# Optimization experiments

Measured on AMD Instinct MI355X. Metric: run time of the kernel, lower is better.

The kernel has to match this reference:

```python
import jax, jax.numpy as jnp
import numpy as np

D_MODEL, D_STATE, D_CONV, EXPAND = 2048, 16, 4, 2
D_INNER = EXPAND * D_MODEL            # 4096
DT_RANK = -(-D_MODEL // 16)           # 128
B_SZ, L = 2, 1024


def setup_inputs() -> dict:
    key = jax.random.key(0)
    ks = jax.random.split(key, 10)
    s = 0.02
    return {
        "hidden_states": jax.random.normal(ks[0], (B_SZ, L, D_MODEL), jnp.float32),
        "in_proj_w": jax.random.normal(ks[1], (2 * D_INNER, D_MODEL), jnp.float32) * s,
        "conv_w": jax.random.normal(ks[2], (D_INNER, D_CONV), jnp.float32) * 0.1,
        "conv_b": jax.random.normal(ks[3], (D_INNER,), jnp.float32) * 0.1,
        "x_proj_w": jax.random.normal(ks[4], (DT_RANK + 2 * D_STATE, D_INNER), jnp.float32) * s,
        "dt_proj_w": jax.random.normal(ks[5], (D_INNER, DT_RANK), jnp.float32) * s,
        "dt_proj_b": jax.random.normal(ks[6], (D_INNER,), jnp.float32) * 0.1 - 4.0,
        "A": -jax.random.uniform(ks[7], (D_INNER, D_STATE), jnp.float32, 1.0, 16.0),
        "D": jnp.ones((D_INNER,), jnp.float32),
        "out_proj_w": jax.random.normal(ks[8], (D_MODEL, D_INNER), jnp.float32) * s,
    }


def _mamba_forward(hidden_states, in_proj_w, conv_w, conv_b, x_proj_w,
                   dt_proj_w, dt_proj_b, A, D, out_proj_w):
    # in_proj: [B,L,d_model] -> [B,L,2*d_inner]; chunk into x and gate
    proj = jnp.einsum('bld,ed->ble', hidden_states, in_proj_w)
    x, gate = jnp.split(proj, 2, axis=-1)            # each [B,L,d_inner]

    # depthwise causal conv1d over time + SiLU
    xc = x.transpose(0, 2, 1)                        # [B,d_inner,L]
    xc = jax.lax.conv_general_dilated(
        xc, conv_w[:, None, :],                      # kernel [d_inner,1,d_conv]
        window_strides=(1,), padding=[(D_CONV - 1, 0)],
        feature_group_count=D_INNER,
        dimension_numbers=('NCH', 'OIH', 'NCH'))
    xc = jax.nn.silu(xc + conv_b[None, :, None])
    xt = xc.transpose(0, 2, 1)                       # [B,L,d_inner]

    # x_proj -> (dt_rank, d_state, d_state)
    ssm = jnp.einsum('bld,ed->ble', xt, x_proj_w)
    ts, Bm, Cm = jnp.split(ssm, [DT_RANK, DT_RANK + D_STATE], axis=-1)
    dt = jnp.einsum('blr,dr->bld', ts, dt_proj_w)    # dt_proj (skip_bias_add)
    dt = jax.nn.softplus(dt + dt_proj_b)             # delta_softplus with bias

    # selective scan over time
    def step(state, inp):
        dt_t, x_t, B_t, C_t = inp                    # [B,di],[B,di],[B,ds],[B,ds]
        dA = jnp.exp(dt_t[..., None] * A)            # [B,d_inner,d_state]
        dBx = dt_t[..., None] * B_t[:, None, :] * x_t[..., None]
        state = state * dA + dBx
        y = jnp.einsum('bds,bs->bd', state, C_t)
        return state, y

    xs = (dt.transpose(1, 0, 2), xt.transpose(1, 0, 2),
          Bm.transpose(1, 0, 2), Cm.transpose(1, 0, 2))
    state0 = jnp.zeros((hidden_states.shape[0], D_INNER, D_STATE), jnp.float32)
    _, ys = jax.lax.scan(step, state0, xs)           # [L,B,d_inner]
    y = ys.transpose(1, 0, 2) + xt * D               # D skip connection
    y = y * jax.nn.silu(gate)                        # gating (z in selective scan)

    return jnp.einsum('bld,ed->ble', y, out_proj_w)  # out_proj -> [B,L,d_model]


def reference(hidden_states, in_proj_w, conv_w, conv_b, x_proj_w,
              dt_proj_w, dt_proj_b, A, D, out_proj_w):
    return _mamba_forward(hidden_states, in_proj_w, conv_w, conv_b, x_proj_w,
                          dt_proj_w, dt_proj_b, A, D, out_proj_w)
```

## Files before the change

kernel.cpp:

```cpp
#include <hip/hip_runtime.h>
#include <hip/hip_bf16.h>
#include <math.h>

#define B_SZ    2
#define LSEQ    1024
#define D_MODEL 2048
#define D_INNER 4096
#define D_STATE 16
#define DT_RANK 128
#define M_TOK   (B_SZ * LSEQ)
#define NCHUNK  16
#define LCHUNK  (LSEQ / NCHUNK)
#define LOG2E   1.4426950408889634f

typedef __attribute__((ext_vector_type(8))) short bf16x8;
typedef __attribute__((ext_vector_type(4))) float f32x4;

__device__ __forceinline__ float softplusf_(float x) {
    return fmaxf(x, 0.f) + log1pf(expf(-fabsf(x)));
}
__device__ __forceinline__ unsigned f2bf(float f) {
    union { float f; unsigned u; } v; v.f = f;
    const unsigned u = v.u;
    return (u + 0x7fffu + ((u >> 16) & 1u)) >> 16;
}
__device__ __forceinline__ float bf2f(unsigned u) {
    union { unsigned u; float f; } v; v.u = u << 16; return v.f;
}
__device__ __forceinline__ void gload16(const void* g, void* lds) {
    __builtin_amdgcn_global_load_lds(
        (const __attribute__((address_space(1))) void*)g,
        (__attribute__((address_space(3))) void*)lds, 16, 0, 0);
}
__device__ __forceinline__ float exp2fast(float x) {
    return __builtin_amdgcn_exp2f(x);
}
__device__ __forceinline__ float sigmoid2(float x) {
    return 1.f / (1.f + exp2fast(-x * LOG2E));
}

__global__ __launch_bounds__(512, 2)
void gemm256_1ph(const ushort* __restrict__ A, int lda,
                 const ushort* __restrict__ B, int ldb,
                 void* __restrict__ Cv, int ldc,
                 void* __restrict__ Cv2,
                 int K, int epi, size_t zstride)
{
    __shared__ ushort Lds[2][2][2][128 * 64];
    const int t    = threadIdx.x;
    const int bm   = blockIdx.y << 8, bn = blockIdx.x << 8;
    const int wave = t >> 6, lane = t & 63;
    const int wm   = wave >> 2;
    const int wn   = wave & 3;
    const int lr   = lane & 15, lh = lane >> 4;
    const int kper  = K / gridDim.z;
    const int kbase = blockIdx.z * kper;
    const int nkt   = kper >> 6;

    const ushort* gsA[2]; const ushort* gsB[2];
    int dof[2];
#pragma unroll
    for (int it = 0; it < 2; ++it) {
        const int flat = t + (it << 9);
        const int row  = flat >> 3, j = flat & 7;
        const int jj   = j ^ (row & 7);
        gsA[it] = A + (size_t)(bm + row) * lda + kbase + jj * 8;
        gsB[it] = B + (size_t)(bn + row) * ldb + kbase + jj * 8;
        dof[it] = flat << 3;
    }

#define STG_A(half, kt, db) do {                                            \
    _Pragma("unroll")                                                       \
    for (int it = 0; it < 2; ++it)                                          \
        gload16(gsA[it] + (size_t)((half) * 128) * lda + (kt) * 64,         \
                &Lds[db][0][half][dof[it]]);                                \
} while (0)
#define STG_B(half, kt, db) do {                                            \
    _Pragma("unroll")                                                       \
    for (int it = 0; it < 2; ++it)                                          \
        gload16(gsB[it] + (size_t)((half) * 128) * ldb + (kt) * 64,         \
                &Lds[db][1][half][dof[it]]);                                \
} while (0)
#define RD_A(db, half) do {                                                 \
    _Pragma("unroll")                                                       \
    for (int mi = 0; mi < 4; ++mi)                                          \
    _Pragma("unroll")                                                       \
    for (int kk = 0; kk < 2; ++kk) {                                        \
        const int row_ = wm * 64 + mi * 16 + lr;                            \
        const int ch_  = ((kk << 2) + lh) ^ (row_ & 7);                     \
        af[mi * 2 + kk] = *(const bf16x8*)((const char*)Lds[db][0][half]    \
                             + row_ * 128 + (ch_ << 4));                    \
    }                                                                       \
} while (0)
#define RD_B(db, half, dst) do {                                            \
    _Pragma("unroll")                                                       \
    for (int nj = 0; nj < 2; ++nj)                                          \
    _Pragma("unroll")                                                       \
    for (int kk = 0; kk < 2; ++kk) {                                        \
        const int row_ = wn * 32 + nj * 16 + lr;                            \
        const int ch_  = ((kk << 2) + lh) ^ (row_ & 7);                     \
        dst[nj * 2 + kk] = *(const bf16x8*)((const char*)Lds[db][1][half]   \
                             + row_ * 128 + (ch_ << 4));                    \
    }                                                                       \
} while (0)
#define MFMA_PAIR(qa, qb, bfa, bfb) do {                                    \
    _Pragma("unroll")                                                       \
    for (int kk = 0; kk < 2; ++kk) {                                        \
        _Pragma("unroll")                                                   \
        for (int mi = 0; mi < 4; ++mi)                                      \
        _Pragma("unroll")                                                   \
        for (int nj = 0; nj < 2; ++nj)                                      \
            acc[qa][mi][nj] = __builtin_amdgcn_mfma_f32_16x16x32_bf16(      \
                af[mi * 2 + kk], bfa[nj * 2 + kk], acc[qa][mi][nj], 0, 0, 0);\
        _Pragma("unroll")                                                   \
        for (int mi = 0; mi < 4; ++mi)                                      \
        _Pragma("unroll")                                                   \
        for (int nj = 0; nj < 2; ++nj)                                      \
            acc[qb][mi][nj] = __builtin_amdgcn_mfma_f32_16x16x32_bf16(      \
                af[mi * 2 + kk], bfb[nj * 2 + kk], acc[qb][mi][nj], 0, 0, 0);\
    }                                                                       \
} while (0)

    f32x4 acc[4][4][2];
#pragma unroll
    for (int q = 0; q < 4; ++q)
#pragma unroll
        for (int i = 0; i < 4; ++i)
#pragma unroll
            for (int j = 0; j < 2; ++j) {
                acc[q][i][j][0] = 0.f; acc[q][i][j][1] = 0.f;
                acc[q][i][j][2] = 0.f; acc[q][i][j][3] = 0.f;
            }

    bf16x8 af[8], bf0[4], bf1[4];

    STG_A(0, 0, 0); STG_B(0, 0, 0); STG_B(1, 0, 0); STG_A(1, 0, 0);
    asm volatile("s_waitcnt vmcnt(0)" ::: "memory");
    __builtin_amdgcn_s_barrier();

    for (int kt = 0; kt < nkt; ++kt) {
        const int db = kt & 1;
        RD_A(db, 0); RD_B(db, 0, bf0); RD_B(db, 1, bf1);
        if (kt + 1 < nkt) {
            STG_A(0, kt + 1, db ^ 1); STG_B(0, kt + 1, db ^ 1);
            STG_B(1, kt + 1, db ^ 1); STG_A(1, kt + 1, db ^ 1);
        }
        MFMA_PAIR(0, 1, bf0, bf1);
        RD_A(db, 1);
        MFMA_PAIR(2, 3, bf1, bf0);
        asm volatile("s_waitcnt vmcnt(0)" ::: "memory");
        __builtin_amdgcn_s_barrier();
    }
#undef STG_A
#undef STG_B
#undef RD_A
#undef RD_B
#undef MFMA_PAIR

    float*  C  = (float*)Cv + (size_t)blockIdx.z * zstride;
    ushort* Cb = (ushort*)Cv;
    ushort* C2 = (ushort*)Cv2;
#pragma unroll
    for (int q = 0; q < 4; ++q) {
        const int mh = q >> 1;
        const int nh = (q == 1 || q == 2) ? 1 : 0;
#pragma unroll
        for (int mi = 0; mi < 4; ++mi) {
#pragma unroll
            for (int nj = 0; nj < 2; ++nj) {
                const int col  = bn + nh * 128 + wn * 32 + nj * 16 + lr;
                const int row0 = bm + mh * 128 + wm * 64 + mi * 16 + (lh << 2);
#pragma unroll
                for (int r = 0; r < 4; ++r) {
                    const float v = acc[q][mi][nj][r];
                    if (epi == 0) {
                        C[(size_t)(row0 + r) * ldc + col] = v;
                    } else {
                        if (col < D_INNER)
                            Cb[(size_t)(row0 + r) * ldc + col] = (ushort)f2bf(v);
                        else
                            C2[(size_t)(row0 + r) * ldc + (col - D_INNER)] = (ushort)f2bf(v);
                    }
                }
            }
        }
    }
}

__global__ __launch_bounds__(512, 4)
void gemm_bf16_bt(const ushort* __restrict__ A, int lda,
                  const ushort* __restrict__ B, int ldb,
                  void* __restrict__ Cv, int ldc,
                  const float* __restrict__ bias,
                  int M, int N, int K, int epi, size_t zstride)
{
    __shared__ ushort As[2][128 * 64];
    __shared__ ushort Bs[2][128 * 64];
    const int t    = threadIdx.x;
    const int bm   = blockIdx.y << 7, bn = blockIdx.x << 7;
    const int wave = t >> 6, lane = t & 63;
    const int wr   = (wave >> 2) << 6;
    const int wc   = (wave & 3) << 5;
    const int lr   = lane & 15, lh = lane >> 4;
    const int kper  = K / gridDim.z;
    const int kbase = blockIdx.z * kper;
    const int nkt   = kper >> 6;

    const ushort* ga[2]; const ushort* gb[2];
    int ldof[2];
#pragma unroll
    for (int it = 0; it < 2; ++it) {
        const int seg = wave + (it << 3);
        const int row = (seg << 3) + (lane >> 3);
        const int jj  = (lane & 7) ^ ((lane >> 3) & 7);
        ga[it] = A + (size_t)(bm + row) * lda + kbase + jj * 8;
        int gn = bn + row; gn = gn < N ? gn : N - 1;
        gb[it] = B + (size_t)gn * ldb + kbase + jj * 8;
        ldof[it] = seg << 9;
    }

#define STAGE(bsel) do {                                                \
    _Pragma("unroll")                                                   \
    for (int it = 0; it < 2; ++it) {                                    \
        gload16(ga[it], &As[bsel][ldof[it]]);                           \
        gload16(gb[it], &Bs[bsel][ldof[it]]);                           \
        ga[it] += 64; gb[it] += 64;                                     \
    }                                                                   \
} while (0)

    f32x4 acc[4][2];
#pragma unroll
    for (int i = 0; i < 4; ++i)
#pragma unroll
        for (int j = 0; j < 2; ++j) {
            acc[i][j][0] = 0.f; acc[i][j][1] = 0.f;
            acc[i][j][2] = 0.f; acc[i][j][3] = 0.f;
        }

    STAGE(0);
    for (int kt = 0; kt < nkt; ++kt) {
        const int cur = kt & 1;
        if (kt + 1 < nkt) {
            STAGE(cur ^ 1);
            asm volatile("s_waitcnt vmcnt(4)" ::: "memory");
        } else {
            asm volatile("s_waitcnt vmcnt(0)" ::: "memory");
        }
        __builtin_amdgcn_s_barrier();

        const char* Ab = (const char*)As[cur];
        const char* Bb = (const char*)Bs[cur];
#pragma unroll
        for (int kk = 0; kk < 2; ++kk) {
            bf16x8 af[4], bf[2];
#pragma unroll
            for (int mi = 0; mi < 4; ++mi) {
                const int row = wr + (mi << 4) + lr;
                const int ch  = ((kk << 2) + lh) ^ (row & 7);
                af[mi] = *(const bf16x8*)(Ab + row * 128 + (ch << 4));
            }
#pragma unroll
            for (int nj = 0; nj < 2; ++nj) {
                const int row = wc + (nj << 4) + lr;
                const int ch  = ((kk << 2) + lh) ^ (row & 7);
                bf[nj] = *(const bf16x8*)(Bb + row * 128 + (ch << 4));
            }
#pragma unroll
            for (int mi = 0; mi < 4; ++mi)
#pragma unroll
                for (int nj = 0; nj < 2; ++nj)
                    acc[mi][nj] = __builtin_amdgcn_mfma_f32_16x16x32_bf16(
                        af[mi], bf[nj], acc[mi][nj], 0, 0, 0);
        }
        __builtin_amdgcn_s_barrier();
    }
#undef STAGE

    float*  C  = (float*)Cv + (size_t)blockIdx.z * zstride;
    ushort* Cb = (ushort*)Cv;
#pragma unroll
    for (int mi = 0; mi < 4; ++mi) {
#pragma unroll
        for (int nj = 0; nj < 2; ++nj) {
            const int col  = bn + wc + (nj << 4) + lr;
            const int row0 = bm + wr + (mi << 4) + (lh << 2);
            if (col < N) {
#pragma unroll
                for (int r = 0; r < 4; ++r) {
                    const float v = acc[mi][nj][r];
                    if (epi == 0)
                        C[(size_t)(row0 + r) * ldc + col] = v;
                    else
                        Cb[(size_t)(row0 + r) * ldc + col] =
                            (ushort)f2bf(softplusf_(v + bias[col]));
                }
            }
        }
    }
}

#define CVT_N_HS   524288
#define CVT_N_INW  2097152
#define CVT1_E0    (CVT_N_HS)
#define CVT1_E1    (CVT1_E0 + CVT_N_INW)

__global__ __launch_bounds__(256)
void cvt_step1(const float* __restrict__ hs,  ushort* __restrict__ hsb,
               const float* __restrict__ inw, ushort* __restrict__ inwb)
{
    for (int i = blockIdx.x * 256 + threadIdx.x; i < CVT1_E1; i += gridDim.x * 256) {
        const float* in; ushort* out; int j;
        if (i < CVT1_E0) { in = hs;  out = hsb;  j = i; }
        else             { in = inw; out = inwb; j = i - CVT1_E0; }
        const float4 v0 = ((const float4*)in)[j * 2];
        const float4 v1 = ((const float4*)in)[j * 2 + 1];
        int4 p;
        p.x = (int)(f2bf(v0.x) | (f2bf(v0.y) << 16));
        p.y = (int)(f2bf(v0.z) | (f2bf(v0.w) << 16));
        p.z = (int)(f2bf(v1.x) | (f2bf(v1.y) << 16));
        p.w = (int)(f2bf(v1.z) | (f2bf(v1.w) << 16));
        ((int4*)out)[j] = p;
    }
}

#define CVT_N_OW   1048576
#define CVT_N_XW   81920
#define CVT_N_DTW  65536
#define CVT4_E0    (CVT_N_OW)
#define CVT4_E1    (CVT4_E0 + CVT_N_XW)
#define CVT4_E2    (CVT4_E1 + CVT_N_DTW)

__global__ __launch_bounds__(256)
void cvt_step4(const float* __restrict__ ow,  ushort* __restrict__ owb,
               const float* __restrict__ xw,  ushort* __restrict__ xwb,
               const float* __restrict__ dtw, ushort* __restrict__ dtwb)
{
    for (int i = blockIdx.x * 256 + threadIdx.x; i < CVT4_E2; i += gridDim.x * 256) {
        const float* in; ushort* out; int j;
        if (i < CVT4_E0)      { in = ow;  out = owb;  j = i; }
        else if (i < CVT4_E1) { in = xw;  out = xwb;  j = i - CVT4_E0; }
        else                  { in = dtw; out = dtwb; j = i - CVT4_E1; }
        const float4 v0 = ((const float4*)in)[j * 2];
        const float4 v1 = ((const float4*)in)[j * 2 + 1];
        int4 p;
        p.x = (int)(f2bf(v0.x) | (f2bf(v0.y) << 16));
        p.y = (int)(f2bf(v0.z) | (f2bf(v0.w) << 16));
        p.z = (int)(f2bf(v1.x) | (f2bf(v1.y) << 16));
        p.w = (int)(f2bf(v1.z) | (f2bf(v1.w) << 16));
        ((int4*)out)[j] = p;
    }
}

__global__ __launch_bounds__(256)
void reduce_out4(const float* __restrict__ part, float* __restrict__ out, int n4)
{
    const int stride = M_TOK * D_MODEL / 4;
    for (int i = blockIdx.x * 256 + threadIdx.x; i < n4; i += gridDim.x * 256) {
        const float4 a = ((const float4*)part)[i];
        const float4 b = ((const float4*)part)[i + stride];
        const float4 c = ((const float4*)part)[i + 2 * stride];
        const float4 d = ((const float4*)part)[i + 3 * stride];
        ((float4*)out)[i] = make_float4(a.x + b.x + c.x + d.x,
                                        a.y + b.y + c.y + d.y,
                                        a.z + b.z + c.z + d.z,
                                        a.w + b.w + c.w + d.w);
    }
}

__global__ __launch_bounds__(256)
void conv_silu_k(const ushort* __restrict__ xraw,
                 const float* __restrict__ cw,
                 const float* __restrict__ cb,
                 ushort* __restrict__ xb)
{
    const int d  = (blockIdx.x << 8) + threadIdx.x;
    const int m0 = blockIdx.y << 6;
    const int l0 = m0 & (LSEQ - 1);
    const float4 w = *(const float4*)&cw[d << 2];
    const float bias = cb[d];
    float x3 = 0.f, x2 = 0.f, x1 = 0.f;
    if (l0 > 0) {
        x3 = bf2f(xraw[(size_t)(m0 - 3) * D_INNER + d]);
        x2 = bf2f(xraw[(size_t)(m0 - 2) * D_INNER + d]);
        x1 = bf2f(xraw[(size_t)(m0 - 1) * D_INNER + d]);
    }
#pragma unroll 4
    for (int i = 0; i < 64; ++i) {
        const size_t m = (size_t)m0 + i;
        const float x0 = bf2f(xraw[m * D_INNER + d]);
        float acc = bias;
        acc = fmaf(w.x, x3, acc);
        acc = fmaf(w.y, x2, acc);
        acc = fmaf(w.z, x1, acc);
        acc = fmaf(w.w, x0, acc);
        xb[m * D_INNER + d] = (ushort)f2bf(acc * sigmoid2(acc));
        x3 = x2; x2 = x1; x1 = x0;
    }
}

__global__ __launch_bounds__(256)
void reduce_ssm(const float* __restrict__ part,
                float* __restrict__ ssmf, ushort* __restrict__ ssmb)
{
    const int i = blockIdx.x * 256 + threadIdx.x;
    float v = 0.f;
#pragma unroll
    for (int z = 0; z < 8; ++z) v += part[(size_t)z * (M_TOK * 160) + i];
    ssmf[i] = v;
    ssmb[i] = (ushort)f2bf(v);
}

__global__ __launch_bounds__(256)
void scan_fused(const ushort* __restrict__ dtp,
                ushort* __restrict__ xb,
                const ushort* __restrict__ gb,
                const float* __restrict__ ssm,
                const float* __restrict__ Ap,
                const float* __restrict__ Dp)
{
    __shared__ float Pl[16 * 17 * 16];
    __shared__ float Ql[16 * 17 * 16];
    const int t  = threadIdx.x;
    const int dl = t & 15, c = t >> 4;
    const int d  = (blockIdx.x << 4) + dl;
    const int b  = blockIdx.y;
    const int base = (dl * 17 + c) * 16;

    float a2[16];
    *(float4*)&a2[0]  = *(const float4*)&Ap[d * 16];
    *(float4*)&a2[4]  = *(const float4*)&Ap[d * 16 + 4];
    *(float4*)&a2[8]  = *(const float4*)&Ap[d * 16 + 8];
    *(float4*)&a2[12] = *(const float4*)&Ap[d * 16 + 12];
#pragma unroll
    for (int s = 0; s < 16; ++s) a2[s] *= LOG2E;
    const size_t m0 = (size_t)b * LSEQ + (size_t)c * LCHUNK;

    float q[16];
#pragma unroll
    for (int s = 0; s < 16; ++s) q[s] = 0.f;
    float dtsum = 0.f;
#pragma unroll 2
    for (int l = 0; l < LCHUNK; ++l) {
        const size_t m = m0 + l;
        const float dt = bf2f(dtp[m * D_INNER + d]);
        const float xv = bf2f(xb[m * D_INNER + d]);
        const float4 B0 = *(const float4*)&ssm[m * 160 + 128];
        const float4 B1 = *(const float4*)&ssm[m * 160 + 132];
        const float4 B2 = *(const float4*)&ssm[m * 160 + 136];
        const float4 B3 = *(const float4*)&ssm[m * 160 + 140];
        const float Bv[16] = {B0.x,B0.y,B0.z,B0.w, B1.x,B1.y,B1.z,B1.w,
                              B2.x,B2.y,B2.z,B2.w, B3.x,B3.y,B3.z,B3.w};
        const float t1 = dt * xv;
#pragma unroll
        for (int s = 0; s < 16; ++s) {
            const float dA = exp2fast(dt * a2[s]);
            q[s] = fmaf(q[s], dA, t1 * Bv[s]);
        }
        dtsum += dt;
    }
#pragma unroll
    for (int s4 = 0; s4 < 4; ++s4) {
        float4 Pv;
        Pv.x = exp2fast(a2[s4 * 4 + 0] * dtsum);
        Pv.y = exp2fast(a2[s4 * 4 + 1] * dtsum);
        Pv.z = exp2fast(a2[s4 * 4 + 2] * dtsum);
        Pv.w = exp2fast(a2[s4 * 4 + 3] * dtsum);
        *(float4*)&Pl[base + s4 * 4] = Pv;
        *(float4*)&Ql[base + s4 * 4] = make_float4(q[s4*4], q[s4*4+1],
                                                   q[s4*4+2], q[s4*4+3]);
    }
    __syncthreads();

    {
        const int dl2 = t >> 4, s2 = t & 15;
        float st2 = 0.f;
#pragma unroll
        for (int c2 = 0; c2 < NCHUNK; ++c2) {
            const int idx = (dl2 * 17 + c2) * 16 + s2;
            const float Pv = Pl[idx];
            const float qv = Ql[idx];
            Ql[idx] = st2;
            st2 = fmaf(st2, Pv, qv);
        }
    }
    __syncthreads();

    float st[16];
#pragma unroll
    for (int s4 = 0; s4 < 4; ++s4)
        *(float4*)&st[s4 * 4] = *(const float4*)&Ql[base + s4 * 4];
    const float Dd = Dp[d];
#pragma unroll 2
    for (int l = 0; l < LCHUNK; ++l) {
        const size_t m = m0 + l;
        const float dt = bf2f(dtp[m * D_INNER + d]);
        const float xv = bf2f(xb[m * D_INNER + d]);
        const float gv = bf2f(gb[m * D_INNER + d]);
        const float4 B0 = *(const float4*)&ssm[m * 160 + 128];
        const float4 B1 = *(const float4*)&ssm[m * 160 + 132];
        const float4 B2 = *(const float4*)&ssm[m * 160 + 136];
        const float4 B3 = *(const float4*)&ssm[m * 160 + 140];
        const float4 C0 = *(const float4*)&ssm[m * 160 + 144];
        const float4 C1 = *(const float4*)&ssm[m * 160 + 148];
        const float4 C2 = *(const float4*)&ssm[m * 160 + 152];
        const float4 C3 = *(const float4*)&ssm[m * 160 + 156];
        const float Bv[16] = {B0.x,B0.y,B0.z,B0.w, B1.x,B1.y,B1.z,B1.w,
                              B2.x,B2.y,B2.z,B2.w, B3.x,B3.y,B3.z,B3.w};
        const float Cv[16] = {C0.x,C0.y,C0.z,C0.w, C1.x,C1.y,C1.z,C1.w,
                              C2.x,C2.y,C2.z,C2.w, C3.x,C3.y,C3.z,C3.w};
        const float t1 = dt * xv;
        float y = 0.f;
#pragma unroll
        for (int s = 0; s < 16; ++s) {
            const float dA = exp2fast(dt * a2[s]);
            st[s] = fmaf(st[s], dA, t1 * Bv[s]);
            y = fmaf(st[s], Cv[s], y);
        }
        const float yg = fmaf(Dd, xv, y);
        xb[m * D_INNER + d] = (ushort)f2bf(yg * (gv * sigmoid2(gv)));
    }
}

extern "C" void kernel_launch(void* const* d_in, const int* in_sizes, int n_in,
                              void* d_out, int out_size, void* d_ws, size_t ws_size,
                              hipStream_t stream)
{
    (void)in_sizes; (void)n_in; (void)out_size; (void)ws_size;
    const float* hs  = (const float*)d_in[0];
    const float* inw = (const float*)d_in[1];
    const float* cw  = (const float*)d_in[2];
    const float* cb  = (const float*)d_in[3];
    const float* xw  = (const float*)d_in[4];
    const float* dtw = (const float*)d_in[5];
    const float* dtb = (const float*)d_in[6];
    const float* Ap  = (const float*)d_in[7];
    const float* Dp  = (const float*)d_in[8];
    const float* ow  = (const float*)d_in[9];
    float* out = (float*)d_out;

    float*  ws    = (float*)d_ws;
    float*  P     = ws;
    ushort* hsb   = (ushort*)(ws + 0);
    ushort* inwb  = (ushort*)(ws + 2097152);
    ushort* dtb16 = (ushort*)(ws + 0);
    ushort* xwb   = (ushort*)(ws + 4194304);
    ushort* dtwb  = (ushort*)(ws + 4521984);
    float*  ssmf  = ws + 4784128;
    ushort* ssmb  = (ushort*)(ws + 5111808);
    float*  part  = ws + 5275648;
    ushort* pg    = (ushort*)(ws + 10485760);
    ushort* xtb   = (ushort*)(ws + 16777216);
    ushort* xraw  = (ushort*)(ws + 20971520);
    ushort* owb   = (ushort*)(ws + 20971520);

    const dim3 blk(256);
    const dim3 blk512(512);

    cvt_step1<<<dim3(2048), blk, 0, stream>>>(hs, hsb, inw, inwb);

    gemm256_1ph<<<dim3(32, 8, 1), blk512, 0, stream>>>(
        hsb, D_MODEL, inwb, D_MODEL, xraw, D_INNER, pg, D_MODEL, 5, 0);

    conv_silu_k<<<dim3(16, 32), blk, 0, stream>>>(xraw, cw, cb, xtb);

    cvt_step4<<<dim3(2048), blk, 0, stream>>>(ow, owb, xw, xwb, dtw, dtwb);

    gemm_bf16_bt<<<dim3(2, 16, 8), blk512, 0, stream>>>(
        xtb, D_INNER, xwb, D_INNER, part, 160, nullptr,
        M_TOK, 160, D_INNER, 0, (size_t)M_TOK * 160);
    reduce_ssm<<<dim3(1280), blk, 0, stream>>>(part, ssmf, ssmb);

    gemm_bf16_bt<<<dim3(32, 16, 1), blk512, 0, stream>>>(
        ssmb, 160, dtwb, DT_RANK, dtb16, D_INNER, dtb,
        M_TOK, D_INNER, DT_RANK, 1, 0);

    scan_fused<<<dim3(D_INNER / 16, B_SZ), blk, 0, stream>>>(
        dtb16, xtb, pg, ssmf, Ap, Dp);

    gemm256_1ph<<<dim3(8, 8, 4), blk512, 0, stream>>>(
        xtb, D_INNER, owb, D_INNER, P, D_MODEL, nullptr,
        D_INNER, 0, (size_t)M_TOK * D_MODEL);
    reduce_out4<<<dim3(1024), blk, 0, stream>>>(P, out, (M_TOK * D_MODEL) / 4);
}
```

Before: 288.0 us.

## Split scan state dimension across two threads per channel in scan_fused

```diff
diff --git a/kernel.cpp b/kernel.cpp
--- a/kernel.cpp
+++ b/kernel.cpp
@@ -418,48 +418,46 @@
                 const float* __restrict__ Ap,
                 const float* __restrict__ Dp)
 {
-    __shared__ float Pl[16 * 17 * 16];
-    __shared__ float Ql[16 * 17 * 16];
+    __shared__ float Pl[8 * 17 * 16];
+    __shared__ float Ql[8 * 17 * 16];
     const int t  = threadIdx.x;
-    const int dl = t & 15, c = t >> 4;
-    const int d  = (blockIdx.x << 4) + dl;
+    const int dl = t & 7;
+    const int sh = (t >> 3) & 1;
+    const int c  = t >> 4;
+    const int d  = (blockIdx.x << 3) + dl;
     const int b  = blockIdx.y;
-    const int base = (dl * 17 + c) * 16;
-
-    float a2[16];
-    *(float4*)&a2[0]  = *(const float4*)&Ap[d * 16];
-    *(float4*)&a2[4]  = *(const float4*)&Ap[d * 16 + 4];
-    *(float4*)&a2[8]  = *(const float4*)&Ap[d * 16 + 8];
-    *(float4*)&a2[12] = *(const float4*)&Ap[d * 16 + 12];
-#pragma unroll
-    for (int s = 0; s < 16; ++s) a2[s] *= LOG2E;
+    const int s0 = sh << 3;
+    const int base = (dl * 17 + c) * 16 + s0;
+
+    float a2[8];
+    *(float4*)&a2[0] = *(const float4*)&Ap[d * 16 + s0];
+    *(float4*)&a2[4] = *(const float4*)&Ap[d * 16 + s0 + 4];
+#pragma unroll
+    for (int s = 0; s < 8; ++s) a2[s] *= LOG2E;
     const size_t m0 = (size_t)b * LSEQ + (size_t)c * LCHUNK;
 
-    float q[16];
-#pragma unroll
-    for (int s = 0; s < 16; ++s) q[s] = 0.f;
+    float q[8];
+#pragma unroll
+    for (int s = 0; s < 8; ++s) q[s] = 0.f;
     float dtsum = 0.f;
 #pragma unroll 2
     for (int l = 0; l < LCHUNK; ++l) {
         const size_t m = m0 + l;
         const float dt = bf2f(dtp[m * D_INNER + d]);
         const float xv = bf2f(xb[m * D_INNER + d]);
-        const float4 B0 = *(const float4*)&ssm[m * 160 + 128];
-        const float4 B1 = *(const float4*)&ssm[m * 160 + 132];
-        const float4 B2 = *(const float4*)&ssm[m * 160 + 136];
-        const float4 B3 = *(const float4*)&ssm[m * 160 + 140];
-        const float Bv[16] = {B0.x,B0.y,B0.z,B0.w, B1.x,B1.y,B1.z,B1.w,
-                              B2.x,B2.y,B2.z,B2.w, B3.x,B3.y,B3.z,B3.w};
+        const float4 B0 = *(const float4*)&ssm[m * 160 + 128 + s0];
+        const float4 B1 = *(const float4*)&ssm[m * 160 + 132 + s0];
+        const float Bv[8] = {B0.x,B0.y,B0.z,B0.w, B1.x,B1.y,B1.z,B1.w};
         const float t1 = dt * xv;
 #pragma unroll
-        for (int s = 0; s < 16; ++s) {
+        for (int s = 0; s < 8; ++s) {
             const float dA = exp2fast(dt * a2[s]);
             q[s] = fmaf(q[s], dA, t1 * Bv[s]);
         }
         dtsum += dt;
     }
 #pragma unroll
-    for (int s4 = 0; s4 < 4; ++s4) {
+    for (int s4 = 0; s4 < 2; ++s4) {
         float4 Pv;
         Pv.x = exp2fast(a2[s4 * 4 + 0] * dtsum);
         Pv.y = exp2fast(a2[s4 * 4 + 1] * dtsum);
@@ -471,7 +469,7 @@
     }
     __syncthreads();
 
-    {
+    if (t < 128) {
         const int dl2 = t >> 4, s2 = t & 15;
         float st2 = 0.f;
 #pragma unroll
@@ -485,10 +483,9 @@
     }
     __syncthreads();
 
-    float st[16];
-#pragma unroll
-    for (int s4 = 0; s4 < 4; ++s4)
-        *(float4*)&st[s4 * 4] = *(const float4*)&Ql[base + s4 * 4];
+    float st[8];
+    *(float4*)&st[0] = *(const float4*)&Ql[base];
+    *(float4*)&st[4] = *(const float4*)&Ql[base + 4];
     const float Dd = Dp[d];
 #pragma unroll 2
     for (int l = 0; l < LCHUNK; ++l) {
@@ -496,28 +493,25 @@
         const float dt = bf2f(dtp[m * D_INNER + d]);
         const float xv = bf2f(xb[m * D_INNER + d]);
         const float gv = bf2f(gb[m * D_INNER + d]);
-        const float4 B0 = *(const float4*)&ssm[m * 160 + 128];
-        const float4 B1 = *(const float4*)&ssm[m * 160 + 132];
-        const float4 B2 = *(const float4*)&ssm[m * 160 + 136];
-        const float4 B3 = *(const float4*)&ssm[m * 160 + 140];
-        const float4 C0 = *(const float4*)&ssm[m * 160 + 144];
-        const float4 C1 = *(const float4*)&ssm[m * 160 + 148];
-        const float4 C2 = *(const float4*)&ssm[m * 160 + 152];
-        const float4 C3 = *(const float4*)&ssm[m * 160 + 156];
-        const float Bv[16] = {B0.x,B0.y,B0.z,B0.w, B1.x,B1.y,B1.z,B1.w,
-                              B2.x,B2.y,B2.z,B2.w, B3.x,B3.y,B3.z,B3.w};
-        const float Cv[16] = {C0.x,C0.y,C0.z,C0.w, C1.x,C1.y,C1.z,C1.w,
-                              C2.x,C2.y,C2.z,C2.w, C3.x,C3.y,C3.z,C3.w};
+        const float4 B0 = *(const float4*)&ssm[m * 160 + 128 + s0];
+        const float4 B1 = *(const float4*)&ssm[m * 160 + 132 + s0];
+        const float4 C0 = *(const float4*)&ssm[m * 160 + 144 + s0];
+        const float4 C1 = *(const float4*)&ssm[m * 160 + 148 + s0];
+        const float Bv[8] = {B0.x,B0.y,B0.z,B0.w, B1.x,B1.y,B1.z,B1.w};
+        const float Cv[8] = {C0.x,C0.y,C0.z,C0.w, C1.x,C1.y,C1.z,C1.w};
         const float t1 = dt * xv;
         float y = 0.f;
 #pragma unroll
-        for (int s = 0; s < 16; ++s) {
+        for (int s = 0; s < 8; ++s) {
             const float dA = exp2fast(dt * a2[s]);
             st[s] = fmaf(st[s], dA, t1 * Bv[s]);
             y = fmaf(st[s], Cv[s], y);
         }
-        const float yg = fmaf(Dd, xv, y);
-        xb[m * D_INNER + d] = (ushort)f2bf(yg * (gv * sigmoid2(gv)));
+        y += __shfl_xor(y, 8);
+        if (sh == 0) {
+            const float yg = fmaf(Dd, xv, y);
+            xb[m * D_INNER + d] = (ushort)f2bf(yg * (gv * sigmoid2(gv)));
+        }
     }
 }
 
@@ -574,7 +568,7 @@
         ssmb, 160, dtwb, DT_RANK, dtb16, D_INNER, dtb,
         M_TOK, D_INNER, DT_RANK, 1, 0);
 
-    scan_fused<<<dim3(D_INNER / 16, B_SZ), blk, 0, stream>>>(
+    scan_fused<<<dim3(D_INNER / 8, B_SZ), blk, 0, stream>>>(
         dtb16, xtb, pg, ssmf, Ap, Dp);
 
     gemm256_1ph<<<dim3(8, 8, 4), blk512, 0, stream>>>(
```

Result: slower. 351.1 us (+21.9%).
